# Optimization experiments

Hardware: AMD Instinct MI355X
Metric: run time of the kernel (lower is better)

The kernel has to match this reference:

```python
import jax, jax.numpy as jnp
import numpy as np

F_SIZE = 256
N_HEAD = 4
D_HEAD = F_SIZE // N_HEAD
B = 16384
E = 31  # number of 'other' entities


def setup_inputs() -> dict:
    key = jax.random.key(0)
    ks = jax.random.split(key, 9)
    s = 1.0 / np.sqrt(F_SIZE)  # ~ nn.Linear init scale
    inp = {
        "ego": jax.random.normal(ks[0], (B, 1, F_SIZE), dtype=jnp.float32),
        "others": jax.random.normal(ks[1], (B, E, F_SIZE), dtype=jnp.float32),
        "mask": jax.random.randint(ks[2], (B, E + 1), 0, 2).astype(bool),
        "Wq": jax.random.uniform(ks[3], (F_SIZE, F_SIZE), jnp.float32, -s, s),
        "Wk": jax.random.uniform(ks[4], (F_SIZE, F_SIZE), jnp.float32, -s, s),
        "Wv": jax.random.uniform(ks[5], (F_SIZE, F_SIZE), jnp.float32, -s, s),
        "Wok": jax.random.uniform(ks[6], (F_SIZE, F_SIZE), jnp.float32, -s, s),
        "Wov": jax.random.uniform(ks[7], (F_SIZE, F_SIZE), jnp.float32, -s, s),
        "Wc": jax.random.uniform(ks[8], (F_SIZE, F_SIZE), jnp.float32, -s, s),
    }
    return inp


def reference(ego, others, mask, Wq, Wk, Wv, Wok, Wov, Wc):
    b = others.shape[0]
    e = others.shape[1]
    # nn.Linear(bias=False): y = x @ W.T
    ego_q = (ego @ Wq.T).reshape(b, 1, N_HEAD, D_HEAD)
    ego_k = (ego @ Wk.T).reshape(b, 1, N_HEAD, D_HEAD)
    ego_v = (ego @ Wv.T).reshape(b, 1, N_HEAD, D_HEAD)
    oth_k = (others @ Wok.T).reshape(b, e, N_HEAD, D_HEAD)
    oth_v = (others @ Wov.T).reshape(b, e, N_HEAD, D_HEAD)
    all_k = jnp.concatenate([ego_k, oth_k], axis=1)  # (b, e+1, h, d)
    all_v = jnp.concatenate([ego_v, oth_v], axis=1)
    # scores: single query per head -> (b, h, 1, e+1)
    scores = jnp.einsum('bqhd,bkhd->bhqk', ego_q, all_k) / np.sqrt(D_HEAD)
    scores = jnp.where(mask[:, None, None, :], jnp.float32(-1e9), scores)
    attn = jax.nn.softmax(scores, axis=-1)
    value = jnp.einsum('bhqk,bkhd->bqhd', attn, all_v).reshape(b, F_SIZE)
    res = ((value @ Wc.T) + ego[:, 0, :]) * 0.5
    return res, attn
```

## Files before the change

### kernel.cpp

```cpp
#include <hip/hip_runtime.h>
#include <hip/hip_bf16.h>

typedef __attribute__((ext_vector_type(8))) short bf16x8;
typedef __attribute__((ext_vector_type(4))) float f32x4;

#define NB 16384
#define NE 31
#define KS_ITEMS 32
#define KS_GRID (NB / KS_ITEMS)

static __device__ __forceinline__ unsigned short f2b(float f) {
  unsigned int u = __builtin_bit_cast(unsigned int, f);
  return (unsigned short)((u + 0x7fffu + ((u >> 16) & 1u)) >> 16);
}
static __device__ __forceinline__ float b2f(unsigned short h) {
  return __builtin_bit_cast(float, ((unsigned int)h) << 16);
}
static __device__ __forceinline__ void gload16(const void* g, void* l) {
  __builtin_amdgcn_global_load_lds(
      (const __attribute__((address_space(1))) void*)g,
      (__attribute__((address_space(3))) void*)l, 16, 0, 0);
}

__global__ void k0_all(const float* __restrict__ wq, const float* __restrict__ wk,
                       const float* __restrict__ wv, const float* __restrict__ wok,
                       const float* __restrict__ wov, const float* __restrict__ wc,
                       unsigned short* __restrict__ W1, unsigned short* __restrict__ W2) {
  int r = blockIdx.x, k = threadIdx.x;
  if (r < 1024) {
    if (r < 256) {
      W1[r * 256 + k] = f2b(0.125f * wq[r * 256 + k]);
    } else if (r < 512) {
      W1[r * 256 + k] = f2b(wk[(r - 256) * 256 + k]);
    } else if (r < 768) {
      W1[r * 256 + k] = f2b(wv[(r - 512) * 256 + k]);
    } else {
      int n = r - 768;
      W2[n * 1280 + 1024 + k] = f2b(wc[n * 256 + k]);
    }
  } else if (r < 2048) {
    int m = r - 1024;
    int h = m >> 8, c = m & 255;
    float acc = 0.f;
#pragma unroll 8
    for (int d = 0; d < 64; ++d)
      acc = fmaf(wq[(h * 64 + d) * 256 + k], wok[(h * 64 + d) * 256 + c], acc);
    W1[(768 + m) * 256 + k] = f2b(0.125f * acc);
  } else {
    int n = r - 2048;
#pragma unroll 1
    for (int mi = 0; mi < 4; ++mi) {
      float acc = 0.f;
#pragma unroll 8
      for (int d = 0; d < 64; ++d)
        acc = fmaf(wov[(mi * 64 + d) * 256 + k], wc[n * 256 + mi * 64 + d], acc);
      W2[n * 1280 + mi * 256 + k] = f2b(acc);
    }
  }
}

__global__ __launch_bounds__(256, 2)
void k1b(const float* __restrict__ ego, const unsigned short* __restrict__ W1,
         unsigned short* __restrict__ qkv2) {
  __shared__ __align__(16) unsigned short Al[64 * 256];
  const int tid = threadIdx.x;
  const int bM = blockIdx.x * 64;
#pragma unroll
  for (int it = 0; it < 8; ++it) {
    int c = tid + it * 256;
    int row = c >> 5, k8 = c & 31;
    const float4* g = (const float4*)(ego + (size_t)(bM + row) * 256 + k8 * 8);
    float4 x = g[0], y = g[1];
    float t[8] = {x.x, x.y, x.z, x.w, y.x, y.y, y.z, y.w};
    bf16x8 v;
#pragma unroll
    for (int j = 0; j < 8; ++j) v[j] = (short)f2b(t[j]);
    int byteoff = row * 512 + ((k8 * 16) ^ ((row & 7) << 4));
    *(bf16x8*)((char*)Al + byteoff) = v;
  }
  __syncthreads();
  const int w = tid >> 6, lane = tid & 63, lr = lane & 15, lkg = lane >> 4;
#pragma unroll 1
  for (int cb = 0; cb < 7; ++cb) {
    int bN = w * 448 + cb * 64;
    f32x4 acc[4][4];
#pragma unroll
    for (int mt = 0; mt < 4; ++mt)
#pragma unroll
      for (int nt = 0; nt < 4; ++nt) acc[mt][nt] = (f32x4){0.f, 0.f, 0.f, 0.f};
#pragma unroll
    for (int kk = 0; kk < 8; ++kk) {
      int kidx = kk * 32 + lkg * 8;
      bf16x8 bfr[4];
#pragma unroll
      for (int nt = 0; nt < 4; ++nt)
        bfr[nt] = *(const bf16x8*)(W1 + (size_t)(bN + nt * 16 + lr) * 256 + kidx);
#pragma unroll
      for (int mt = 0; mt < 4; ++mt) {
        int row = mt * 16 + lr;
        int byteoff = row * 512 + ((kidx * 2) ^ ((row & 7) << 4));
        bf16x8 a = *(const bf16x8*)((const char*)Al + byteoff);
#pragma unroll
        for (int nt = 0; nt < 4; ++nt)
          acc[mt][nt] = __builtin_amdgcn_mfma_f32_16x16x32_bf16(a, bfr[nt], acc[mt][nt], 0, 0, 0);
      }
    }
#pragma unroll
    for (int mt = 0; mt < 4; ++mt)
#pragma unroll
      for (int nt = 0; nt < 4; ++nt)
#pragma unroll
        for (int j = 0; j < 4; ++j) {
          int row = bM + mt * 16 + lkg * 4 + j;
          int col = bN + nt * 16 + lr;
          qkv2[(size_t)row * 1792 + col] = f2b(acc[mt][nt][j]);
        }
  }
}

__global__ __launch_bounds__(256, 2)
void ks_attn(const float* __restrict__ others, const int* __restrict__ mask,
             const unsigned short* __restrict__ qkv2,
             unsigned short* __restrict__ u,
             float* __restrict__ attnout) {
  __shared__ __align__(16) float Xf[2][32 * 256];
  __shared__ __align__(16) unsigned short Qb[2][2048];
  __shared__ float sco_l[4][32];
  __shared__ float Pl[4][32];
  const int tid = threadIdx.x;
  const int w = tid >> 6, lane = tid & 63, lr = lane & 15, lkg = lane >> 4;
  const size_t b0 = (size_t)blockIdx.x * KS_ITEMS;

  auto issue = [&](int buf, size_t bb) {
#pragma unroll 1
    for (int t = w; t < 35; t += 4) {
      if (t < 31) {
        const char* g = (const char*)(others + (bb * 31 + t) * 256) +
                        ((lane * 16) ^ ((t & 7) << 4));
        gload16(g, (char*)&Xf[buf][t * 256]);
      } else {
        int t2 = t - 31;
        const char* g = (const char*)(qkv2 + bb * 1792 + t2 * 512) + lane * 16;
        gload16(g, (char*)&Qb[buf][t2 * 512]);
      }
    }
  };

  issue(0, b0);
  asm volatile("s_waitcnt vmcnt(0)" ::: "memory");
  __builtin_amdgcn_s_barrier();
  __builtin_amdgcn_sched_barrier(0);

#pragma unroll 1
  for (int it = 0; it < KS_ITEMS; ++it) {
    const size_t bb = b0 + it;
    const int cur = it & 1;
    if (it + 1 < KS_ITEMS) issue(cur ^ 1, bb + 1);

    const float* X = Xf[cur];
    const unsigned short* Q = Qb[cur];

    if (w < 2) {
      f32x4 acc = (f32x4){0.f, 0.f, 0.f, 0.f};
      const int r = w * 16 + lr;
      const int sw = (r & 7) << 4;
      const char* xrow = (const char*)X + r * 1024;
#pragma unroll
      for (int kk = 0; kk < 8; ++kk) {
        bf16x8 a = *(const bf16x8*)(&Q[768 + (lr & 3) * 256 + kk * 32 + lkg * 8]);
        int cb = kk * 128 + lkg * 32;
        float4 x0 = *(const float4*)(xrow + (cb ^ sw));
        float4 x1 = *(const float4*)(xrow + ((cb + 16) ^ sw));
        bf16x8 bfr;
        bfr[0] = (short)f2b(x0.x); bfr[1] = (short)f2b(x0.y);
        bfr[2] = (short)f2b(x0.z); bfr[3] = (short)f2b(x0.w);
        bfr[4] = (short)f2b(x1.x); bfr[5] = (short)f2b(x1.y);
        bfr[6] = (short)f2b(x1.z); bfr[7] = (short)f2b(x1.w);
        acc = __builtin_amdgcn_mfma_f32_16x16x32_bf16(a, bfr, acc, 0, 0, 0);
      }
      if (lkg == 0) {
        int n = w * 16 + lr;
        if (n < NE) {
#pragma unroll
          for (int j = 0; j < 4; ++j) sco_l[j][1 + n] = acc[j];
        }
      }
    } else if (w == 2) {
      int h = lane >> 4, i = lane & 15;
      float s = 0.f;
#pragma unroll
      for (int j = 0; j < 4; ++j)
        s += b2f(Q[h * 64 + i * 4 + j]) * b2f(Q[256 + h * 64 + i * 4 + j]);
#pragma unroll
      for (int off = 1; off < 16; off <<= 1) s += __shfl_xor(s, off, 16);
      if (i == 0) sco_l[h][0] = s;
    }
    asm volatile("s_waitcnt lgkmcnt(0)" ::: "memory");
    __builtin_amdgcn_s_barrier();
    __builtin_amdgcn_sched_barrier(0);

    {
      int key = lane & 31;
      float s = sco_l[w][key];
      if (mask[bb * 32 + key] != 0) s = -1e9f;
      float mx = s;
#pragma unroll
      for (int off = 1; off < 32; off <<= 1) mx = fmaxf(mx, __shfl_xor(mx, off, 32));
      float ex = __expf(s - mx);
      float sm = ex;
#pragma unroll
      for (int off = 1; off < 32; off <<= 1) sm += __shfl_xor(sm, off, 32);
      float p = ex / sm;
      if (lane < 32) {
        Pl[w][key] = p;
        attnout[bb * 128 + w * 32 + key] = p;
      }
    }

    {
      float a0 = 0.f, a1 = 0.f, a2 = 0.f, a3 = 0.f;
#pragma unroll
      for (int e = 0; e < NE; ++e) {
        float p = Pl[w][1 + e];
        float4 xv = *(const float4*)((const char*)X + e * 1024 +
                                     ((lane * 16) ^ ((e & 7) << 4)));
        a0 = fmaf(p, xv.x, a0);
        a1 = fmaf(p, xv.y, a1);
        a2 = fmaf(p, xv.z, a2);
        a3 = fmaf(p, xv.w, a3);
      }
      ushort4 st;
      st.x = f2b(a0); st.y = f2b(a1); st.z = f2b(a2); st.w = f2b(a3);
      *(ushort4*)(u + bb * 1280 + w * 256 + lane * 4) = st;
      float p0 = Pl[w][0];
      u[bb * 1280 + 1024 + w * 64 + lane] = f2b(p0 * b2f(Q[512 + w * 64 + lane]));
    }

    asm volatile("s_waitcnt vmcnt(0)" ::: "memory");
    __builtin_amdgcn_s_barrier();
    __builtin_amdgcn_sched_barrier(0);
  }
}

__global__ __launch_bounds__(256, 2)
void k4_out(const unsigned short* __restrict__ u, const unsigned short* __restrict__ W2,
            const float* __restrict__ ego, float* __restrict__ out) {
  __shared__ __align__(16) unsigned short Au[32 * 256];
  const int tid = threadIdx.x;
  const int bM = blockIdx.x * 32;
  const int w = tid >> 6, lane = tid & 63, lr = lane & 15, lkg = lane >> 4;
  f32x4 acc[2][4];
#pragma unroll
  for (int mt = 0; mt < 2; ++mt)
#pragma unroll
    for (int nt = 0; nt < 4; ++nt) acc[mt][nt] = (f32x4){0.f, 0.f, 0.f, 0.f};
#pragma unroll 1
  for (int kc = 0; kc < 5; ++kc) {
#pragma unroll
    for (int it = 0; it < 4; ++it) {
      int c = tid + it * 256;
      int row = c >> 5, k8 = c & 31;
      bf16x8 v = *(const bf16x8*)(u + (size_t)(bM + row) * 1280 + kc * 256 + k8 * 8);
      int byteoff = row * 512 + ((k8 * 16) ^ ((row & 7) << 4));
      *(bf16x8*)((char*)Au + byteoff) = v;
    }
    __syncthreads();
#pragma unroll
    for (int kk = 0; kk < 8; ++kk) {
      int kidx = kk * 32 + lkg * 8;
      bf16x8 bfr[4];
#pragma unroll
      for (int nt = 0; nt < 4; ++nt)
        bfr[nt] = *(const bf16x8*)(W2 + (size_t)(w * 64 + nt * 16 + lr) * 1280 + kc * 256 + kidx);
#pragma unroll
      for (int mt = 0; mt < 2; ++mt) {
        int row = mt * 16 + lr;
        int byteoff = row * 512 + ((kidx * 2) ^ ((row & 7) << 4));
        bf16x8 a = *(const bf16x8*)((const char*)Au + byteoff);
#pragma unroll
        for (int nt = 0; nt < 4; ++nt)
          acc[mt][nt] = __builtin_amdgcn_mfma_f32_16x16x32_bf16(a, bfr[nt], acc[mt][nt], 0, 0, 0);
      }
    }
    __syncthreads();
  }
#pragma unroll
  for (int mt = 0; mt < 2; ++mt)
#pragma unroll
    for (int nt = 0; nt < 4; ++nt)
#pragma unroll
      for (int j = 0; j < 4; ++j) {
        int row = bM + mt * 16 + lkg * 4 + j;
        int col = w * 64 + nt * 16 + lr;
        out[(size_t)row * 256 + col] = (acc[mt][nt][j] + ego[(size_t)row * 256 + col]) * 0.5f;
      }
}

extern "C" void kernel_launch(void* const* d_in, const int* in_sizes, int n_in,
                              void* d_out, int out_size, void* d_ws, size_t ws_size,
                              hipStream_t stream) {
  const float* ego    = (const float*)d_in[0];
  const float* others = (const float*)d_in[1];
  const int*   mask   = (const int*)d_in[2];
  const float* wq  = (const float*)d_in[3];
  const float* wk  = (const float*)d_in[4];
  const float* wv  = (const float*)d_in[5];
  const float* wok = (const float*)d_in[6];
  const float* wov = (const float*)d_in[7];
  const float* wc  = (const float*)d_in[8];

  unsigned short* W1   = (unsigned short*)d_ws;
  unsigned short* W2   = W1 + 1792 * 256;
  unsigned short* qkv2 = W2 + 256 * 1280;
  unsigned short* u    = qkv2 + (size_t)NB * 1792;

  float* res  = (float*)d_out;
  float* attn = res + (size_t)NB * 256;

  hipLaunchKernelGGL(k0_all, dim3(2304), dim3(256), 0, stream,
                     wq, wk, wv, wok, wov, wc, W1, W2);
  hipLaunchKernelGGL(k1b,    dim3(256),  dim3(256), 0, stream, ego, W1, qkv2);
  hipLaunchKernelGGL(ks_attn, dim3(KS_GRID), dim3(256), 0, stream,
                     others, mask, qkv2, u, attn);
  hipLaunchKernelGGL(k4_out, dim3(512),  dim3(256), 0, stream, u, W2, ego, res);
}
```

Before: 281.0 us.

## Assign one batch item per wavefront in attention kernel with bf16 LDS staging

The attention kernel no longer walks 32 items per block through a double-buffered async global-to-LDS pipeline with block-wide barriers. Each wavefront now handles one batch item independently. It loads the others rows to registers, converts them to bf16 with a packed cvt instruction and stores them swizzled in LDS, then runs score MFMAs, a per-wave softmax and a p·X reduction for all 4 heads. This removes block barriers and the idle waves of the old w<2 / w==2 split, and halves LDS footprint. The cost is losing explicit prefetch overlap, so latency hiding depends on occupancy across many small blocks.

```diff
diff --git a/kernel.cpp b/kernel.cpp
--- a/kernel.cpp
+++ b/kernel.cpp
@@ -6,8 +6,6 @@
 
 #define NB 16384
 #define NE 31
-#define KS_ITEMS 32
-#define KS_GRID (NB / KS_ITEMS)
 
 static __device__ __forceinline__ unsigned short f2b(float f) {
   unsigned int u = __builtin_bit_cast(unsigned int, f);
@@ -16,10 +14,10 @@
 static __device__ __forceinline__ float b2f(unsigned short h) {
   return __builtin_bit_cast(float, ((unsigned int)h) << 16);
 }
-static __device__ __forceinline__ void gload16(const void* g, void* l) {
-  __builtin_amdgcn_global_load_lds(
-      (const __attribute__((address_space(1))) void*)g,
-      (__attribute__((address_space(3))) void*)l, 16, 0, 0);
+static __device__ __forceinline__ unsigned int cvtpk(float a, float b) {
+  unsigned int r;
+  asm("v_cvt_pk_bf16_f32 %0, %1, %2" : "=v"(r) : "v"(a), "v"(b));
+  return r;
 }
 
 __global__ void k0_all(const float* __restrict__ wq, const float* __restrict__ wk,
@@ -123,123 +121,134 @@
              const unsigned short* __restrict__ qkv2,
              unsigned short* __restrict__ u,
              float* __restrict__ attnout) {
-  __shared__ __align__(16) float Xf[2][32 * 256];
-  __shared__ __align__(16) unsigned short Qb[2][2048];
-  __shared__ float sco_l[4][32];
-  __shared__ float Pl[4][32];
+  __shared__ __align__(16) unsigned short Xs[4][8192];
+  __shared__ __align__(16) float Ps[4][32][4];
   const int tid = threadIdx.x;
   const int w = tid >> 6, lane = tid & 63, lr = lane & 15, lkg = lane >> 4;
-  const size_t b0 = (size_t)blockIdx.x * KS_ITEMS;
-
-  auto issue = [&](int buf, size_t bb) {
-#pragma unroll 1
-    for (int t = w; t < 35; t += 4) {
-      if (t < 31) {
-        const char* g = (const char*)(others + (bb * 31 + t) * 256) +
-                        ((lane * 16) ^ ((t & 7) << 4));
-        gload16(g, (char*)&Xf[buf][t * 256]);
-      } else {
-        int t2 = t - 31;
-        const char* g = (const char*)(qkv2 + bb * 1792 + t2 * 512) + lane * 16;
-        gload16(g, (char*)&Qb[buf][t2 * 512]);
-      }
-    }
-  };
-
-  issue(0, b0);
-  asm volatile("s_waitcnt vmcnt(0)" ::: "memory");
-  __builtin_amdgcn_s_barrier();
+  const size_t b = (size_t)blockIdx.x * 4 + w;
+  char* Xc = (char*)Xs[w];
+  float (*P)[4] = Ps[w];
+  const unsigned short* qk = qkv2 + b * 1792;
+
+  bf16x8 af[8];
+#pragma unroll
+  for (int kk = 0; kk < 8; ++kk)
+    af[kk] = *(const bf16x8*)(qk + 768 + (lr & 3) * 256 + kk * 32 + lkg * 8);
+  ushort4 qa = *(const ushort4*)(qk + lkg * 64 + lr * 4);
+  ushort4 kb = *(const ushort4*)(qk + 256 + lkg * 64 + lr * 4);
+  ushort4 ve = *(const ushort4*)(qk + 512 + lane * 4);
+  int mk0 = mask[b * 32 + 1 + lr];
+  int mk1 = (lr == 15) ? 1 : mask[b * 32 + 17 + lr];
+  int mkE = mask[b * 32];
+
+  {
+    const char* src = (const char*)(others + b * (NE * 256)) + lane * 16;
+#pragma unroll
+    for (int j = 0; j < 31; ++j) {
+      float4 f = *(const float4*)(src + j * 1024);
+      uint2 v;
+      v.x = cvtpk(f.x, f.y);
+      v.y = cvtpk(f.z, f.w);
+      *(uint2*)(Xc + j * 512 + ((lane * 8) ^ ((j & 15) << 4))) = v;
+    }
+    uint2 z; z.x = 0; z.y = 0;
+    *(uint2*)(Xc + 31 * 512 + ((lane * 8) ^ ((31 & 15) << 4))) = z;
+  }
+
+  float s0p = b2f(qa.x) * b2f(kb.x) + b2f(qa.y) * b2f(kb.y) +
+              b2f(qa.z) * b2f(kb.z) + b2f(qa.w) * b2f(kb.w);
+#pragma unroll
+  for (int off = 1; off < 16; off <<= 1) s0p += __shfl_xor(s0p, off, 16);
+  float s0h[4];
+  s0h[0] = __shfl(s0p, 0);
+  s0h[1] = __shfl(s0p, 16);
+  s0h[2] = __shfl(s0p, 32);
+  s0h[3] = __shfl(s0p, 48);
+
+  asm volatile("s_waitcnt lgkmcnt(0)" ::: "memory");
   __builtin_amdgcn_sched_barrier(0);
 
-#pragma unroll 1
-  for (int it = 0; it < KS_ITEMS; ++it) {
-    const size_t bb = b0 + it;
-    const int cur = it & 1;
-    if (it + 1 < KS_ITEMS) issue(cur ^ 1, bb + 1);
-
-    const float* X = Xf[cur];
-    const unsigned short* Q = Qb[cur];
-
-    if (w < 2) {
-      f32x4 acc = (f32x4){0.f, 0.f, 0.f, 0.f};
-      const int r = w * 16 + lr;
-      const int sw = (r & 7) << 4;
-      const char* xrow = (const char*)X + r * 1024;
-#pragma unroll
-      for (int kk = 0; kk < 8; ++kk) {
-        bf16x8 a = *(const bf16x8*)(&Q[768 + (lr & 3) * 256 + kk * 32 + lkg * 8]);
-        int cb = kk * 128 + lkg * 32;
-        float4 x0 = *(const float4*)(xrow + (cb ^ sw));
-        float4 x1 = *(const float4*)(xrow + ((cb + 16) ^ sw));
-        bf16x8 bfr;
-        bfr[0] = (short)f2b(x0.x); bfr[1] = (short)f2b(x0.y);
-        bfr[2] = (short)f2b(x0.z); bfr[3] = (short)f2b(x0.w);
-        bfr[4] = (short)f2b(x1.x); bfr[5] = (short)f2b(x1.y);
-        bfr[6] = (short)f2b(x1.z); bfr[7] = (short)f2b(x1.w);
-        acc = __builtin_amdgcn_mfma_f32_16x16x32_bf16(a, bfr, acc, 0, 0, 0);
-      }
-      if (lkg == 0) {
-        int n = w * 16 + lr;
-        if (n < NE) {
-#pragma unroll
-          for (int j = 0; j < 4; ++j) sco_l[j][1 + n] = acc[j];
-        }
-      }
-    } else if (w == 2) {
-      int h = lane >> 4, i = lane & 15;
-      float s = 0.f;
-#pragma unroll
-      for (int j = 0; j < 4; ++j)
-        s += b2f(Q[h * 64 + i * 4 + j]) * b2f(Q[256 + h * 64 + i * 4 + j]);
-#pragma unroll
-      for (int off = 1; off < 16; off <<= 1) s += __shfl_xor(s, off, 16);
-      if (i == 0) sco_l[h][0] = s;
-    }
-    asm volatile("s_waitcnt lgkmcnt(0)" ::: "memory");
-    __builtin_amdgcn_s_barrier();
-    __builtin_amdgcn_sched_barrier(0);
-
-    {
-      int key = lane & 31;
-      float s = sco_l[w][key];
-      if (mask[bb * 32 + key] != 0) s = -1e9f;
-      float mx = s;
-#pragma unroll
-      for (int off = 1; off < 32; off <<= 1) mx = fmaxf(mx, __shfl_xor(mx, off, 32));
-      float ex = __expf(s - mx);
-      float sm = ex;
-#pragma unroll
-      for (int off = 1; off < 32; off <<= 1) sm += __shfl_xor(sm, off, 32);
-      float p = ex / sm;
-      if (lane < 32) {
-        Pl[w][key] = p;
-        attnout[bb * 128 + w * 32 + key] = p;
-      }
-    }
-
-    {
-      float a0 = 0.f, a1 = 0.f, a2 = 0.f, a3 = 0.f;
-#pragma unroll
-      for (int e = 0; e < NE; ++e) {
-        float p = Pl[w][1 + e];
-        float4 xv = *(const float4*)((const char*)X + e * 1024 +
-                                     ((lane * 16) ^ ((e & 7) << 4)));
-        a0 = fmaf(p, xv.x, a0);
-        a1 = fmaf(p, xv.y, a1);
-        a2 = fmaf(p, xv.z, a2);
-        a3 = fmaf(p, xv.w, a3);
-      }
-      ushort4 st;
-      st.x = f2b(a0); st.y = f2b(a1); st.z = f2b(a2); st.w = f2b(a3);
-      *(ushort4*)(u + bb * 1280 + w * 256 + lane * 4) = st;
-      float p0 = Pl[w][0];
-      u[bb * 1280 + 1024 + w * 64 + lane] = f2b(p0 * b2f(Q[512 + w * 64 + lane]));
-    }
-
-    asm volatile("s_waitcnt vmcnt(0)" ::: "memory");
-    __builtin_amdgcn_s_barrier();
-    __builtin_amdgcn_sched_barrier(0);
-  }
+  f32x4 acc0 = (f32x4){0.f, 0.f, 0.f, 0.f};
+  f32x4 acc1 = (f32x4){0.f, 0.f, 0.f, 0.f};
+#pragma unroll
+  for (int kk = 0; kk < 8; ++kk) {
+    int co = kk * 64 + lkg * 16;
+    bf16x8 b0 = *(const bf16x8*)(Xc + lr * 512 + (co ^ (lr << 4)));
+    bf16x8 b1 = *(const bf16x8*)(Xc + (16 + lr) * 512 + (co ^ (lr << 4)));
+    acc0 = __builtin_amdgcn_mfma_f32_16x16x32_bf16(af[kk], b0, acc0, 0, 0, 0);
+    acc1 = __builtin_amdgcn_mfma_f32_16x16x32_bf16(af[kk], b1, acc1, 0, 0, 0);
+  }
+
+  float pr0[4], pr1[4], p0v[4];
+#pragma unroll
+  for (int j = 0; j < 4; ++j) {
+    float sj0 = mk0 ? -1e9f : acc0[j];
+    float sj1 = mk1 ? -1e9f : acc1[j];
+    float se  = mkE ? -1e9f : s0h[j];
+    float mx = fmaxf(se, fmaxf(sj0, sj1));
+#pragma unroll
+    for (int off = 1; off < 16; off <<= 1) mx = fmaxf(mx, __shfl_xor(mx, off, 16));
+    float e0 = __expf(sj0 - mx), e1 = __expf(sj1 - mx), ee = __expf(se - mx);
+    float sm = e0 + e1;
+#pragma unroll
+    for (int off = 1; off < 16; off <<= 1) sm += __shfl_xor(sm, off, 16);
+    float rinv = 1.f / (sm + ee);
+    pr0[j] = e0 * rinv;
+    pr1[j] = e1 * rinv;
+    p0v[j] = ee * rinv;
+  }
+  if (lkg == 0) {
+    float4 q0, q1;
+    q0.x = pr0[0]; q0.y = pr0[1]; q0.z = pr0[2]; q0.w = pr0[3];
+    *(float4*)&P[1 + lr][0] = q0;
+    if (lr < 15) {
+      q1.x = pr1[0]; q1.y = pr1[1]; q1.z = pr1[2]; q1.w = pr1[3];
+      *(float4*)&P[17 + lr][0] = q1;
+    }
+    if (lr == 0) {
+      float4 qe;
+      qe.x = p0v[0]; qe.y = p0v[1]; qe.z = p0v[2]; qe.w = p0v[3];
+      *(float4*)&P[0][0] = qe;
+    }
+#pragma unroll
+    for (int j = 0; j < 4; ++j) {
+      attnout[b * 128 + j * 32 + 1 + lr] = pr0[j];
+      if (lr < 15) attnout[b * 128 + j * 32 + 17 + lr] = pr1[j];
+      if (lr == 0) attnout[b * 128 + j * 32] = p0v[j];
+    }
+  }
+  asm volatile("s_waitcnt lgkmcnt(0)" ::: "memory");
+  __builtin_amdgcn_sched_barrier(0);
+
+  f32x4 cx[4];
+#pragma unroll
+  for (int h = 0; h < 4; ++h) cx[h] = (f32x4){0.f, 0.f, 0.f, 0.f};
+#pragma unroll
+  for (int e = 0; e < NE; ++e) {
+    float4 p = *(const float4*)&P[1 + e][0];
+    ushort4 xv = *(const ushort4*)(Xc + e * 512 + ((lane * 8) ^ ((e & 15) << 4)));
+    float x0 = b2f(xv.x), x1 = b2f(xv.y), x2 = b2f(xv.z), x3 = b2f(xv.w);
+    cx[0][0] = fmaf(p.x, x0, cx[0][0]); cx[0][1] = fmaf(p.x, x1, cx[0][1]);
+    cx[0][2] = fmaf(p.x, x2, cx[0][2]); cx[0][3] = fmaf(p.x, x3, cx[0][3]);
+    cx[1][0] = fmaf(p.y, x0, cx[1][0]); cx[1][1] = fmaf(p.y, x1, cx[1][1]);
+    cx[1][2] = fmaf(p.y, x2, cx[1][2]); cx[1][3] = fmaf(p.y, x3, cx[1][3]);
+    cx[2][0] = fmaf(p.z, x0, cx[2][0]); cx[2][1] = fmaf(p.z, x1, cx[2][1]);
+    cx[2][2] = fmaf(p.z, x2, cx[2][2]); cx[2][3] = fmaf(p.z, x3, cx[2][3]);
+    cx[3][0] = fmaf(p.w, x0, cx[3][0]); cx[3][1] = fmaf(p.w, x1, cx[3][1]);
+    cx[3][2] = fmaf(p.w, x2, cx[3][2]); cx[3][3] = fmaf(p.w, x3, cx[3][3]);
+  }
+#pragma unroll
+  for (int h = 0; h < 4; ++h) {
+    ushort4 st;
+    st.x = f2b(cx[h][0]); st.y = f2b(cx[h][1]);
+    st.z = f2b(cx[h][2]); st.w = f2b(cx[h][3]);
+    *(ushort4*)(u + b * 1280 + h * 256 + lane * 4) = st;
+  }
+  float p0h = P[0][lkg];
+  ushort4 sv;
+  sv.x = f2b(p0h * b2f(ve.x)); sv.y = f2b(p0h * b2f(ve.y));
+  sv.z = f2b(p0h * b2f(ve.z)); sv.w = f2b(p0h * b2f(ve.w));
+  *(ushort4*)(u + b * 1280 + 1024 + lane * 4) = sv;
 }
 
 __global__ __launch_bounds__(256, 2)
@@ -320,7 +329,7 @@
   hipLaunchKernelGGL(k0_all, dim3(2304), dim3(256), 0, stream,
                      wq, wk, wv, wok, wov, wc, W1, W2);
   hipLaunchKernelGGL(k1b,    dim3(256),  dim3(256), 0, stream, ego, W1, qkv2);
-  hipLaunchKernelGGL(ks_attn, dim3(KS_GRID), dim3(256), 0, stream,
+  hipLaunchKernelGGL(ks_attn, dim3(NB / 4), dim3(256), 0, stream,
                      others, mask, qkv2, u, attn);
   hipLaunchKernelGGL(k4_out, dim3(512),  dim3(256), 0, stream, u, W2, ego, res);
 }
```

New measurement: 254.4 us. 1.1x faster.
